# Kernel optimization log

Hardware: AMD Instinct MI355X
Metric: run time of the kernel (lower is better)

## Reference

```python
import jax, jax.numpy as jnp
import numpy as np

B, T, V, E, H = 256, 512, 50000, 300, 128
NORM_GAIN = 0.8     # norm_gain fed at train time
FORGET_BIAS = 1.0
EPS = 1e-12         # tf.contrib.layers.layer_norm default epsilon


def setup_inputs() -> dict:
    key = jax.random.key(0)
    k1, k2, k3 = jax.random.split(key, 3)
    x = jax.random.randint(k1, (B, T), 0, V, dtype=jnp.int32)
    embed = jax.random.normal(k2, (V, E), dtype=jnp.float32)  # tf.random_normal stddev=1
    W = jax.random.normal(k3, (E + H, 4 * H), dtype=jnp.float32) / np.float32(np.sqrt(E + H))
    gains = jnp.full((5, H), NORM_GAIN, dtype=jnp.float32)   # i, j, f, o, cell-transform
    shifts = jnp.zeros((5, H), dtype=jnp.float32)
    return {"x": x, "embed": embed, "W": W, "gains": gains, "shifts": shifts}


def _ln(v, g, b):
    # layer norm over feature axis with learned gain/shift
    m = jnp.mean(v, axis=-1, keepdims=True)
    var = jnp.mean(jnp.square(v - m), axis=-1, keepdims=True)
    return (v - m) * jax.lax.rsqrt(var + EPS) * g + b


def reference(x, embed, W, gains, shifts):
    # embedding: einsum('abc,cd->abd', one_hot(x), embed) == embed[x]
    xe = jnp.take(embed, x, axis=0)            # [B, T, E]
    xe = jnp.transpose(xe, (1, 0, 2))          # [T, B, E] for scan
    c0 = jnp.zeros((x.shape[0], H), jnp.float32)
    h0 = c0

    def step(carry, x_t):
        c, h = carry
        z = jnp.concatenate([x_t, h], axis=-1) @ W      # [B, 4H], no bias
        i, j, f, o = jnp.split(z, 4, axis=-1)
        i = _ln(i, gains[0], shifts[0])
        j = _ln(j, gains[1], shifts[1])
        f = _ln(f, gains[2], shifts[2])
        o = _ln(o, gains[3], shifts[3])
        g = jax.nn.relu(j)                              # activation=tf.nn.relu
        new_c = c * jax.nn.sigmoid(f + FORGET_BIAS) + jax.nn.sigmoid(i) * g
        new_h = jax.nn.relu(_ln(new_c, gains[4], shifts[4])) * jax.nn.sigmoid(o)
        return (new_c, new_h), new_h

    _, ys = jax.lax.scan(step, (c0, h0), xe)            # ys: [T, B, H]
    return jnp.transpose(ys, (1, 0, 2))                 # [B, T, H]
```

## Files before the change

### kernel.cpp

```cpp
#include <hip/hip_runtime.h>
#include <math.h>

#define Bb   256
#define Tt   512
#define Vv   50000
#define Ee   300
#define Hh   128
#define G4   512
#define EPS  1e-12f
#define FBIAS 1.0f

typedef _Float16 half8 __attribute__((ext_vector_type(8)));
typedef float    f32x4 __attribute__((ext_vector_type(4)));

template <int CTRL>
__device__ inline float dpp_mov(float v) {
    return __int_as_float(
        __builtin_amdgcn_update_dpp(0, __float_as_int(v), CTRL, 0xF, 0xF, true));
}
__device__ inline float red16(float v) {
    v += dpp_mov<0xB1>(v);
    v += dpp_mov<0x4E>(v);
    v += dpp_mov<0x141>(v);
    v += dpp_mov<0x140>(v);
    return v;
}
__device__ inline float red64b(float v) {
    v = red16(v);
    v += dpp_mov<0x142>(v);
    v += dpp_mov<0x143>(v);
    return __int_as_float(__builtin_amdgcn_readlane(__float_as_int(v), 63));
}

__device__ inline void lds_barrier() {
    __builtin_amdgcn_sched_barrier(0);
    asm volatile("s_waitcnt lgkmcnt(0)" ::: "memory");
    __builtin_amdgcn_sched_barrier(0);
    __builtin_amdgcn_s_barrier();
    __builtin_amdgcn_sched_barrier(0);
}

__device__ inline float sigm(float v) {
    return __fdividef(1.0f, 1.0f + __expf(-v));
}

#define PROJ_TILES ((Vv + 31) / 32)

__global__ __launch_bounds__(512, 2) void embed_proj_mfma(
    const float* __restrict__ embed,
    const float* __restrict__ W,
    float* __restrict__ P)
{
    __shared__ __align__(16) _Float16 A[32 * 320];

    const int tid  = threadIdx.x;
    const int wv   = tid >> 6;
    const int lane = tid & 63;
    const int p16  = lane & 15;
    const int gq   = lane >> 4;

    half8 bf[4][10];
    #pragma unroll
    for (int tt = 0; tt < 4; ++tt) {
        #pragma unroll
        for (int ks = 0; ks < 10; ++ks) {
            half8 h;
            #pragma unroll
            for (int j = 0; j < 8; ++j) {
                int k = ks * 32 + gq * 8 + j;
                h[j] = (k < Ee)
                     ? (_Float16)W[(size_t)k * G4 + wv * 64 + tt * 16 + p16]
                     : (_Float16)0.f;
            }
            bf[tt][ks] = h;
        }
    }

    char* const Ab = (char*)A;
    for (int i = tid; i < 32 * 10; i += 512) {
        int row = i / 10, m = i - row * 10;
        *(uint*)(Ab + ((row * 640 + 600 + m * 4) ^ ((row & 7) << 4))) = 0u;
    }
    __syncthreads();

    for (int mtile = blockIdx.x; mtile < PROJ_TILES; mtile += gridDim.x) {
        const int r0 = mtile * 32;

        for (int i = tid; i < 32 * 75; i += 512) {
            int row = i / 75, k4 = i - row * 75;
            int grow = r0 + row;
            float4 v = (grow < Vv) ? *(const float4*)&embed[(size_t)grow * Ee + k4 * 4]
                                   : (float4){0.f, 0.f, 0.f, 0.f};
            union { _Float16 h[4]; uint2 u; } pk;
            pk.h[0] = (_Float16)v.x; pk.h[1] = (_Float16)v.y;
            pk.h[2] = (_Float16)v.z; pk.h[3] = (_Float16)v.w;
            *(uint2*)(Ab + ((row * 640 + k4 * 8) ^ ((row & 7) << 4))) = pk.u;
        }
        __syncthreads();

        f32x4 acc[2][4];
        #pragma unroll
        for (int mt = 0; mt < 2; ++mt)
            #pragma unroll
            for (int tt = 0; tt < 4; ++tt)
                acc[mt][tt] = (f32x4){0.f, 0.f, 0.f, 0.f};

        #pragma unroll
        for (int mt = 0; mt < 2; ++mt) {
            const int arow = mt * 16 + p16;
            #pragma unroll
            for (int ks = 0; ks < 10; ++ks) {
                half8 af = *(const half8*)(Ab + ((arow * 640 + ks * 64 + gq * 16)
                                                 ^ ((arow & 7) << 4)));
                #pragma unroll
                for (int tt = 0; tt < 4; ++tt)
                    acc[mt][tt] = __builtin_amdgcn_mfma_f32_16x16x32_f16(
                        af, bf[tt][ks], acc[mt][tt], 0, 0, 0);
            }
        }

        #pragma unroll
        for (int mt = 0; mt < 2; ++mt)
            #pragma unroll
            for (int tt = 0; tt < 4; ++tt)
                #pragma unroll
                for (int r = 0; r < 4; ++r) {
                    int row = r0 + mt * 16 + gq * 4 + r;
                    if (row < Vv)
                        P[(size_t)row * G4 + wv * 64 + tt * 16 + p16] = acc[mt][tt][r];
                }
        __syncthreads();
    }
}

#define RPBLK 4
#define LBLK  (Bb / RPBLK)

#define LSTM_STEP(TSTEP, PC, PN)                                               \
{                                                                              \
                      \
    {                                                                          \
        int tn   = ((TSTEP) + 1 < Tt) ? (TSTEP) + 1 : Tt - 1;                  \
        int tokn = xrow[tn];                                                   \
        _Pragma("unroll")                                                      \
        for (int g = 0; g < 4; ++g)                                            \
            PN[g] = *(const float2*)&P[(size_t)tokn * G4 + g * 128 + 2 * lane];\
    }                                                                          \
    {                                                                          \
        half8 af[4];                                                           \
        _Pragma("unroll")                                                      \
        for (int ks = 0; ks < 4; ++ks)                                         \
            af[ks] = *(const half8*)(hb + p16 * 256 +                          \
                         ((ks * 64 + (gq << 4)) ^ ((p16 & 7) << 4)));          \
        f32x4 acc[8];                                                          \
        _Pragma("unroll")                                                      \
        for (int tt = 0; tt < 8; ++tt) acc[tt] = (f32x4){0.f, 0.f, 0.f, 0.f};  \
        _Pragma("unroll")                                                      \
        for (int tt = 0; tt < 8; ++tt) {                                       \
            _Pragma("unroll")                                                  \
            for (int ks = 0; ks < 4; ++ks)                                     \
                acc[tt] = __builtin_amdgcn_mfma_f32_16x16x32_f16(              \
                    af[ks], bfrag[tt][ks], acc[tt], 0, 0, 0);                  \
        }                                                                      \
        if (lane < 16) {                                                       \
            _Pragma("unroll")                                                  \
            for (int g = 0; g < 4; ++g) {                                      \
                _Pragma("unroll")                                              \
                for (int hh = 0; hh < 2; ++hh) {                               \
                    const int tt  = g * 2 + hh;                                \
                    const int col = g * 128 + wv * 32 + hh * 16 + p16;         \
                    _Pragma("unroll")                                          \
                    for (int r = 0; r < 4; ++r) z_lds[r][col] = acc[tt][r];    \
                }                                                              \
            }                                                                  \
        }                                                                      \
    }                                                                          \
    lds_barrier();                                               \
          \
    {                                                                          \
        float2 zi[4];                                                          \
        _Pragma("unroll")                                                      \
        for (int g = 0; g < 4; ++g) {                                          \
            float2 zr = *(const float2*)&z_lds[wv][g * 128 + 2 * lane];        \
            zi[g].x = zr.x + PC[g].x;                                          \
            zi[g].y = zr.y + PC[g].y;                                          \
        }                                                                      \
        float mean[4], rstd[4];                                                \
        _Pragma("unroll")                                                      \
        for (int g = 0; g < 4; ++g) {                                          \
            float s = red64b(zi[g].x + zi[g].y);                               \
            float q = red64b(fmaf(zi[g].x, zi[g].x, zi[g].y * zi[g].y));       \
            mean[g] = s * (1.0f / Hh);                                         \
            float var = q * (1.0f / Hh) - mean[g] * mean[g];                   \
            rstd[g] = rsqrtf(var + EPS);                                       \
        }                                                                      \
        float2 nv[4];                                                          \
        _Pragma("unroll")                                                      \
        for (int g = 0; g < 4; ++g) {                                          \
            nv[g].x = (zi[g].x - mean[g]) * rstd[g] * gg[g].x + sg[g].x;       \
            nv[g].y = (zi[g].y - mean[g]) * rstd[g] * gg[g].y + sg[g].y;       \
        }                                                                      \
        c0 = c0 * sigm(nv[2].x + FBIAS) + sigm(nv[0].x) * fmaxf(nv[1].x, 0.f); \
        c1 = c1 * sigm(nv[2].y + FBIAS) + sigm(nv[0].y) * fmaxf(nv[1].y, 0.f); \
        float s2 = red64b(c0 + c1);                                            \
        float q2 = red64b(fmaf(c0, c0, c1 * c1));                              \
        const float m2 = s2 * (1.0f / Hh);                                     \
        const float v2 = q2 * (1.0f / Hh) - m2 * m2;                           \
        const float r2 = rsqrtf(v2 + EPS);                                     \
        const float lc0 = (c0 - m2) * r2 * gcell.x + scell.x;                  \
        const float lc1 = (c1 - m2) * r2 * gcell.y + scell.y;                  \
        const float h0 = fmaxf(lc0, 0.f) * sigm(nv[3].x);                      \
        const float h1 = fmaxf(lc1, 0.f) * sigm(nv[3].y);                      \
        {                                                                      \
            union { _Float16 hh2[2]; uint u; } pk;                             \
            pk.hh2[0] = (_Float16)h0; pk.hh2[1] = (_Float16)h1;                \
            *(uint*)(hb + wv * 256 + ((4 * lane) ^ ((wv & 7) << 4))) = pk.u;   \
        }                                                                      \
        *(float2*)&out[((size_t)row_g * Tt + (TSTEP)) * Hh + 2 * lane] =       \
            (float2){h0, h1};                                                  \
    }                                                                          \
    lds_barrier();                                                \
}

__global__ __launch_bounds__(256, 1) void lstm_mfma4(
    const float* __restrict__ P,
    const float* __restrict__ W,
    const int*   __restrict__ x,
    const float* __restrict__ gains,
    const float* __restrict__ shifts,
    float* __restrict__ out)
{
    __shared__ __align__(16) float    z_lds[RPBLK][G4];
    __shared__ __align__(16) _Float16 h_lds[16][Hh];

    const int tid  = threadIdx.x;
    const int wv   = tid >> 6;
    const int lane = tid & 63;
    const int gq   = lane >> 4;
    const int p16  = lane & 15;
    const int bb   = blockIdx.x;

    {
        uint* hz = (uint*)h_lds;
        #pragma unroll
        for (int i = 0; i < 4; ++i) hz[tid + 256 * i] = 0u;
    }

    half8 bfrag[8][4];
    #pragma unroll
    for (int g = 0; g < 4; ++g) {
        #pragma unroll
        for (int hh = 0; hh < 2; ++hh) {
            #pragma unroll
            for (int ks = 0; ks < 4; ++ks) {
                half8 h;
                #pragma unroll
                for (int j = 0; j < 8; ++j) {
                    h[j] = (_Float16)W[(size_t)(Ee + ks * 32 + gq * 8 + j) * G4
                                       + g * 128 + wv * 32 + hh * 16 + p16];
                }
                bfrag[g * 2 + hh][ks] = h;
            }
        }
    }

    float2 gg[4], sg[4];
    #pragma unroll
    for (int g = 0; g < 4; ++g) {
        gg[g] = *(const float2*)&gains[g * Hh + 2 * lane];
        sg[g] = *(const float2*)&shifts[g * Hh + 2 * lane];
    }
    const float2 gcell = *(const float2*)&gains[4 * Hh + 2 * lane];
    const float2 scell = *(const float2*)&shifts[4 * Hh + 2 * lane];

    const int  row_g = bb * RPBLK + wv;
    const int* xrow  = x + (size_t)row_g * Tt;

    float c0 = 0.f, c1 = 0.f;

    float2 pA[4], pB[4];
    {
        int tok0 = xrow[0];
        #pragma unroll
        for (int g = 0; g < 4; ++g)
            pA[g] = *(const float2*)&P[(size_t)tok0 * G4 + g * 128 + 2 * lane];
    }

    char* const hb = (char*)h_lds;

    __syncthreads();

    for (int t = 0; t < Tt; t += 2) {
        LSTM_STEP(t,     pA, pB)
        LSTM_STEP(t + 1, pB, pA)
    }
}

extern "C" void kernel_launch(void* const* d_in, const int* in_sizes, int n_in,
                              void* d_out, int out_size, void* d_ws, size_t ws_size,
                              hipStream_t stream) {
    const int*   x      = (const int*)d_in[0];
    const float* embed  = (const float*)d_in[1];
    const float* W      = (const float*)d_in[2];
    const float* gains  = (const float*)d_in[3];
    const float* shifts = (const float*)d_in[4];
    float* out = (float*)d_out;

    float* P = (float*)d_ws;

    embed_proj_mfma<<<dim3(256), dim3(512), 0, stream>>>(embed, W, P);
    lstm_mfma4<<<dim3(LBLK), dim3(256), 0, stream>>>(P, W, x, gains, shifts, out);
}
```

Measured before the change: 826.7 us.

## Store input projection in fp16, stage tokens in LDS, prefetch two steps ahead

The embedding-projection table P is now written in fp16, which halves both its write traffic and the per-step gather reads in the recurrent kernel. Each block copies its token ids into shared memory up front, so the token lookup no longer touches global memory inside the recurrence. The P rows are prefetched two steps ahead using a three-buffer rotation, which hides gather latency behind more work. The cost is extra rounding on the precomputed input projection and more register and LDS use.

```diff
diff --git a/kernel.cpp b/kernel.cpp
--- a/kernel.cpp
+++ b/kernel.cpp
@@ -49,7 +49,7 @@
 __global__ __launch_bounds__(512, 2) void embed_proj_mfma(
     const float* __restrict__ embed,
     const float* __restrict__ W,
-    float* __restrict__ P)
+    _Float16* __restrict__ P)
 {
     __shared__ __align__(16) _Float16 A[32 * 320];
 
@@ -127,7 +127,8 @@
                 for (int r = 0; r < 4; ++r) {
                     int row = r0 + mt * 16 + gq * 4 + r;
                     if (row < Vv)
-                        P[(size_t)row * G4 + wv * 64 + tt * 16 + p16] = acc[mt][tt][r];
+                        P[(size_t)row * G4 + wv * 64 + tt * 16 + p16] =
+                            (_Float16)acc[mt][tt][r];
                 }
         __syncthreads();
     }
@@ -136,15 +137,14 @@
 #define RPBLK 4
 #define LBLK  (Bb / RPBLK)
 
-#define LSTM_STEP(TSTEP, PC, PN)                                               \
+#define LSTM_STEP(TSTEP, PC, PL)                                               \
 {                                                                              \
-                      \
+              \
     {                                                                          \
-        int tn   = ((TSTEP) + 1 < Tt) ? (TSTEP) + 1 : Tt - 1;                  \
-        int tokn = xrow[tn];                                                   \
+        const _Float16* pr = P + (size_t)tkR * G4;                             \
         _Pragma("unroll")                                                      \
         for (int g = 0; g < 4; ++g)                                            \
-            PN[g] = *(const float2*)&P[(size_t)tokn * G4 + g * 128 + 2 * lane];\
+            PL[g] = *(const uint*)&pr[g * 128 + 2 * lane];                     \
     }                                                                          \
     {                                                                          \
         half8 af[4];                                                           \
@@ -178,12 +178,14 @@
     lds_barrier();                                               \
           \
     {                                                                          \
+        tkR = xtok[wv][((TSTEP) + 3 < Tt) ? (TSTEP) + 3 : Tt - 1];             \
         float2 zi[4];                                                          \
         _Pragma("unroll")                                                      \
         for (int g = 0; g < 4; ++g) {                                          \
+            union { uint u; _Float16 h[2]; } pk; pk.u = PC[g];                 \
             float2 zr = *(const float2*)&z_lds[wv][g * 128 + 2 * lane];        \
-            zi[g].x = zr.x + PC[g].x;                                          \
-            zi[g].y = zr.y + PC[g].y;                                          \
+            zi[g].x = zr.x + (float)pk.h[0];                                   \
+            zi[g].y = zr.y + (float)pk.h[1];                                   \
         }                                                                      \
         float mean[4], rstd[4];                                                \
         _Pragma("unroll")                                                      \
@@ -222,8 +224,8 @@
     lds_barrier();                                                \
 }
 
-__global__ __launch_bounds__(256, 1) void lstm_mfma4(
-    const float* __restrict__ P,
+__global__ __launch_bounds__(256, 1) void lstm_mfma5(
+    const _Float16* __restrict__ P,
     const float* __restrict__ W,
     const int*   __restrict__ x,
     const float* __restrict__ gains,
@@ -232,6 +234,7 @@
 {
     __shared__ __align__(16) float    z_lds[RPBLK][G4];
     __shared__ __align__(16) _Float16 h_lds[16][Hh];
+    __shared__ __align__(16) int      xtok[RPBLK][Tt];
 
     const int tid  = threadIdx.x;
     const int wv   = tid >> 6;
@@ -239,6 +242,12 @@
     const int gq   = lane >> 4;
     const int p16  = lane & 15;
     const int bb   = blockIdx.x;
+
+    {
+        const int4* xs = (const int4*)(x + (size_t)bb * RPBLK * Tt);
+        int4* xd = (int4*)&xtok[0][0];
+        for (int i = tid; i < 512; i += 256) xd[i] = xs[i];
+    }
 
     {
         uint* hz = (uint*)h_lds;
@@ -273,27 +282,35 @@
     const float2 gcell = *(const float2*)&gains[4 * Hh + 2 * lane];
     const float2 scell = *(const float2*)&shifts[4 * Hh + 2 * lane];
 
-    const int  row_g = bb * RPBLK + wv;
-    const int* xrow  = x + (size_t)row_g * Tt;
+    const int row_g = bb * RPBLK + wv;
 
     float c0 = 0.f, c1 = 0.f;
-
-    float2 pA[4], pB[4];
+    char* const hb = (char*)h_lds;
+
+    __syncthreads();
+
+    uint pA[4], pB[4], pC[4];
+    int tkR;
     {
-        int tok0 = xrow[0];
-        #pragma unroll
-        for (int g = 0; g < 4; ++g)
-            pA[g] = *(const float2*)&P[(size_t)tok0 * G4 + g * 128 + 2 * lane];
-    }
-
-    char* const hb = (char*)h_lds;
-
-    __syncthreads();
-
-    for (int t = 0; t < Tt; t += 2) {
-        LSTM_STEP(t,     pA, pB)
+        int tk0 = xtok[wv][0];
+        int tk1 = xtok[wv][1];
+        tkR = xtok[wv][2];
+        const _Float16* p0 = P + (size_t)tk0 * G4;
+        const _Float16* p1 = P + (size_t)tk1 * G4;
+        #pragma unroll
+        for (int g = 0; g < 4; ++g) {
+            pA[g] = *(const uint*)&p0[g * 128 + 2 * lane];
+            pB[g] = *(const uint*)&p1[g * 128 + 2 * lane];
+        }
+    }
+
+    for (int t = 0; t < 510; t += 3) {
+        LSTM_STEP(t,     pA, pC)
         LSTM_STEP(t + 1, pB, pA)
-    }
+        LSTM_STEP(t + 2, pC, pB)
+    }
+    LSTM_STEP(510, pA, pC)
+    LSTM_STEP(511, pB, pA)
 }
 
 extern "C" void kernel_launch(void* const* d_in, const int* in_sizes, int n_in,
@@ -306,8 +323,8 @@
     const float* shifts = (const float*)d_in[4];
     float* out = (float*)d_out;
 
-    float* P = (float*)d_ws;
+    _Float16* P = (_Float16*)d_ws;
 
     embed_proj_mfma<<<dim3(256), dim3(512), 0, stream>>>(embed, W, P);
-    lstm_mfma4<<<dim3(LBLK), dim3(256), 0, stream>>>(P, W, x, gains, shifts, out);
-}
+    lstm_mfma5<<<dim3(LBLK), dim3(256), 0, stream>>>(P, W, x, gains, shifts, out);
+}
```

Result: faster. 794.2 us (-3.9%).

## Split LSTM gate matmul across eight waves with fp16 projection table and fused LN stats

Applied to the files above, without the earlier changes.

The recurrent kernel now runs 512 threads per block, so each of eight waves computes one 64-column gate slice of the h·W product. The per-token input projection is injected directly as the MFMA accumulator initializer, and the projection table is stored as fp16 to halve gather bandwidth. Layer-norm sums and sums of squares are computed from the accumulators and shared via a small LDS partial buffer, which replaces the cross-lane reductions for the four gates. Tokens are staged in LDS, gathers are prefetched two steps ahead, and sched barriers are removed around the block barrier. The cost is lower precision in the projection, extra LDS traffic, and only half the waves doing the elementwise phase.

```diff
diff --git a/kernel.cpp b/kernel.cpp
--- a/kernel.cpp
+++ b/kernel.cpp
@@ -33,11 +33,8 @@
 }
 
 __device__ inline void lds_barrier() {
-    __builtin_amdgcn_sched_barrier(0);
     asm volatile("s_waitcnt lgkmcnt(0)" ::: "memory");
-    __builtin_amdgcn_sched_barrier(0);
     __builtin_amdgcn_s_barrier();
-    __builtin_amdgcn_sched_barrier(0);
 }
 
 __device__ inline float sigm(float v) {
@@ -49,7 +46,7 @@
 __global__ __launch_bounds__(512, 2) void embed_proj_mfma(
     const float* __restrict__ embed,
     const float* __restrict__ W,
-    float* __restrict__ P)
+    _Float16* __restrict__ P)
 {
     __shared__ __align__(16) _Float16 A[32 * 320];
 
@@ -127,7 +124,8 @@
                 for (int r = 0; r < 4; ++r) {
                     int row = r0 + mt * 16 + gq * 4 + r;
                     if (row < Vv)
-                        P[(size_t)row * G4 + wv * 64 + tt * 16 + p16] = acc[mt][tt][r];
+                        P[(size_t)row * G4 + wv * 64 + tt * 16 + p16] =
+                            (_Float16)acc[mt][tt][r];
                 }
         __syncthreads();
     }
@@ -136,70 +134,121 @@
 #define RPBLK 4
 #define LBLK  (Bb / RPBLK)
 
-#define LSTM_STEP(TSTEP, PC, PN)                                               \
+#define PLOAD(PM, TI)                                                          \
 {                                                                              \
-                      \
-    {                                                                          \
-        int tn   = ((TSTEP) + 1 < Tt) ? (TSTEP) + 1 : Tt - 1;                  \
-        int tokn = xrow[tn];                                                   \
-        _Pragma("unroll")                                                      \
-        for (int g = 0; g < 4; ++g)                                            \
-            PN[g] = *(const float2*)&P[(size_t)tokn * G4 + g * 128 + 2 * lane];\
+    const int ti_ = (TI) < Tt ? (TI) : Tt - 1;                                 \
+    const int a0 = xtok[0][ti_], a1 = xtok[1][ti_];                            \
+    const int a2 = xtok[2][ti_], a3 = xtok[3][ti_];                            \
+    const unsigned short* Pu = (const unsigned short*)P;                       \
+    const unsigned short* b0 = Pu + (size_t)a0 * G4 + wv * 64 + p16;           \
+    const unsigned short* b1 = Pu + (size_t)a1 * G4 + wv * 64 + p16;           \
+    const unsigned short* b2 = Pu + (size_t)a2 * G4 + wv * 64 + p16;           \
+    const unsigned short* b3 = Pu + (size_t)a3 * G4 + wv * 64 + p16;           \
+    _Pragma("unroll")                                                          \
+    for (int tt = 0; tt < 4; ++tt) {                                           \
+        PM[0 * 4 + tt] = b0[tt * 16];                                          \
+        PM[1 * 4 + tt] = b1[tt * 16];                                          \
+        PM[2 * 4 + tt] = b2[tt * 16];                                          \
+        PM[3 * 4 + tt] = b3[tt * 16];                                          \
     }                                                                          \
+}
+
+#define LSTM_STEP(TSTEP, PM)                                                   \
+{                                                                              \
+    \
     {                                                                          \
         half8 af[4];                                                           \
         _Pragma("unroll")                                                      \
         for (int ks = 0; ks < 4; ++ks)                                         \
             af[ks] = *(const half8*)(hb + p16 * 256 +                          \
                          ((ks * 64 + (gq << 4)) ^ ((p16 & 7) << 4)));          \
-        f32x4 acc[8];                                                          \
-        _Pragma("unroll")                                                      \
-        for (int tt = 0; tt < 8; ++tt) acc[tt] = (f32x4){0.f, 0.f, 0.f, 0.f};  \
-        _Pragma("unroll")                                                      \
-        for (int tt = 0; tt < 8; ++tt) {                                       \
+        f32x4 acc[4];                                                          \
+        _Pragma("unroll")                                                      \
+        for (int tt = 0; tt < 4; ++tt) {                                       \
+            f32x4 a;                                                           \
+            _Pragma("unroll")                                                  \
+            for (int r = 0; r < 4; ++r) {                                      \
+                unsigned short u = (unsigned short)PM[r * 4 + tt];             \
+                float pv = (float)__builtin_bit_cast(_Float16, u);             \
+                a[r] = (lane < 16) ? pv : 0.f;                                 \
+            }                                                                  \
+            acc[tt] = a;                                                       \
+        }                                                                      \
+        _Pragma("unroll")                                                      \
+        for (int tt = 0; tt < 4; ++tt) {                                       \
             _Pragma("unroll")                                                  \
             for (int ks = 0; ks < 4; ++ks)                                     \
                 acc[tt] = __builtin_amdgcn_mfma_f32_16x16x32_f16(              \
                     af[ks], bfrag[tt][ks], acc[tt], 0, 0, 0);                  \
         }                                                                      \
+                   \
+        PLOAD(PM, (TSTEP) + 2)                                                 \
+                                       \
         if (lane < 16) {                                                       \
             _Pragma("unroll")                                                  \
-            for (int g = 0; g < 4; ++g) {                                      \
+            for (int tt = 0; tt < 4; ++tt) {                                   \
+                const int col = wv * 64 + tt * 16 + p16;                       \
                 _Pragma("unroll")                                              \
-                for (int hh = 0; hh < 2; ++hh) {                               \
-                    const int tt  = g * 2 + hh;                                \
-                    const int col = g * 128 + wv * 32 + hh * 16 + p16;         \
-                    _Pragma("unroll")                                          \
-                    for (int r = 0; r < 4; ++r) z_lds[r][col] = acc[tt][r];    \
-                }                                                              \
+                for (int r = 0; r < 4; ++r) z_lds[r][col] = acc[tt][r];        \
             }                                                                  \
         }                                                                      \
+                 \
+        {                                                                      \
+            float sA[4], qA[4];                                                \
+            _Pragma("unroll")                                                  \
+            for (int r = 0; r < 4; ++r) {                                      \
+                float s = (acc[0][r] + acc[1][r]) + (acc[2][r] + acc[3][r]);   \
+                float q = acc[0][r] * acc[0][r];                               \
+                q = fmaf(acc[1][r], acc[1][r], q);                             \
+                q = fmaf(acc[2][r], acc[2][r], q);                             \
+                q = fmaf(acc[3][r], acc[3][r], q);                             \
+                sA[r] = red16(s); qA[r] = red16(q);                            \
+            }                                                                  \
+            float ws = sA[0], wq = qA[0];                                      \
+            ws = (p16 == 1) ? sA[1] : ws;  wq = (p16 == 1) ? qA[1] : wq;       \
+            ws = (p16 == 2) ? sA[2] : ws;  wq = (p16 == 2) ? qA[2] : wq;       \
+            ws = (p16 == 3) ? sA[3] : ws;  wq = (p16 == 3) ? qA[3] : wq;       \
+            if (lane < 4) *(float2*)&part[lane][wv][0] = (float2){ws, wq};     \
+        }                                                                      \
     }                                                                          \
-    lds_barrier();                                               \
-          \
-    {                                                                          \
+    lds_barrier();                                    \
+             \
+    if (wv < 4) {                                                              \
         float2 zi[4];                                                          \
         _Pragma("unroll")                                                      \
+        for (int g = 0; g < 4; ++g)                                            \
+            zi[g] = *(const float2*)&z_lds[wv][g * 128 + 2 * lane];            \
+        const float4 pt0 = *(const float4*)&part[wv][0][0];                    \
+        const float4 pt1 = *(const float4*)&part[wv][2][0];                    \
+        const float4 pt2 = *(const float4*)&part[wv][4][0];                    \
+        const float4 pt3 = *(const float4*)&part[wv][6][0];                    \
+        float mean[4], rstd[4];                                                \
+        {                                                                      \
+            float st, qt;                                                      \
+            st = pt0.x + pt0.z; qt = pt0.y + pt0.w;                            \
+            mean[0] = st * (1.0f / Hh);                                        \
+            rstd[0] = rsqrtf(qt * (1.0f / Hh) - mean[0] * mean[0] + EPS);      \
+            st = pt1.x + pt1.z; qt = pt1.y + pt1.w;                            \
+            mean[1] = st * (1.0f / Hh);                                        \
+            rstd[1] = rsqrtf(qt * (1.0f / Hh) - mean[1] * mean[1] + EPS);      \
+            st = pt2.x + pt2.z; qt = pt2.y + pt2.w;                            \
+            mean[2] = st * (1.0f / Hh);                                        \
+            rstd[2] = rsqrtf(qt * (1.0f / Hh) - mean[2] * mean[2] + EPS);      \
+            st = pt3.x + pt3.z; qt = pt3.y + pt3.w;                            \
+            mean[3] = st * (1.0f / Hh);                                        \
+            rstd[3] = rsqrtf(qt * (1.0f / Hh) - mean[3] * mean[3] + EPS);      \
+        }                                                                      \
+        float2 nv[4];                                                          \
+        _Pragma("unroll")                                                      \
         for (int g = 0; g < 4; ++g) {                                          \
-            float2 zr = *(const float2*)&z_lds[wv][g * 128 + 2 * lane];        \
-            zi[g].x = zr.x + PC[g].x;                                          \
-            zi[g].y = zr.y + PC[g].y;                                          \
-        }                                                                      \
-        float mean[4], rstd[4];                                                \
-        _Pragma("unroll")                                                      \
-        for (int g = 0; g < 4; ++g) {                                          \
-            float s = red64b(zi[g].x + zi[g].y);                               \
-            float q = red64b(fmaf(zi[g].x, zi[g].x, zi[g].y * zi[g].y));       \
-            mean[g] = s * (1.0f / Hh);                                         \
-            float var = q * (1.0f / Hh) - mean[g] * mean[g];                   \
-            rstd[g] = rsqrtf(var + EPS);                                       \
-        }                                                                      \
-        float2 nv[4];                                                          \
-        _Pragma("unroll")                                                      \
-        for (int g = 0; g < 4; ++g) {                                          \
-            nv[g].x = (zi[g].x - mean[g]) * rstd[g] * gg[g].x + sg[g].x;       \
-            nv[g].y = (zi[g].y - mean[g]) * rstd[g] * gg[g].y + sg[g].y;       \
-        }                                                                      \
+            const float ax = rstd[g] * gg[g].x, ay = rstd[g] * gg[g].y;        \
+            const float bx = sg[g].x - mean[g] * ax;                           \
+            const float by = sg[g].y - mean[g] * ay;                           \
+            nv[g].x = fmaf(zi[g].x, ax, bx);                                   \
+            nv[g].y = fmaf(zi[g].y, ay, by);                                   \
+        }                                                                      \
+        const float sox = sigm(nv[3].x);                                       \
+        const float soy = sigm(nv[3].y);                                       \
         c0 = c0 * sigm(nv[2].x + FBIAS) + sigm(nv[0].x) * fmaxf(nv[1].x, 0.f); \
         c1 = c1 * sigm(nv[2].y + FBIAS) + sigm(nv[0].y) * fmaxf(nv[1].y, 0.f); \
         float s2 = red64b(c0 + c1);                                            \
@@ -209,8 +258,8 @@
         const float r2 = rsqrtf(v2 + EPS);                                     \
         const float lc0 = (c0 - m2) * r2 * gcell.x + scell.x;                  \
         const float lc1 = (c1 - m2) * r2 * gcell.y + scell.y;                  \
-        const float h0 = fmaxf(lc0, 0.f) * sigm(nv[3].x);                      \
-        const float h1 = fmaxf(lc1, 0.f) * sigm(nv[3].y);                      \
+        const float h0 = fmaxf(lc0, 0.f) * sox;                                \
+        const float h1 = fmaxf(lc1, 0.f) * soy;                                \
         {                                                                      \
             union { _Float16 hh2[2]; uint u; } pk;                             \
             pk.hh2[0] = (_Float16)h0; pk.hh2[1] = (_Float16)h1;                \
@@ -222,8 +271,8 @@
     lds_barrier();                                                \
 }
 
-__global__ __launch_bounds__(256, 1) void lstm_mfma4(
-    const float* __restrict__ P,
+__global__ __launch_bounds__(512, 1) void lstm_mfma8(
+    const _Float16* __restrict__ P,
     const float* __restrict__ W,
     const int*   __restrict__ x,
     const float* __restrict__ gains,
@@ -232,6 +281,8 @@
 {
     __shared__ __align__(16) float    z_lds[RPBLK][G4];
     __shared__ __align__(16) _Float16 h_lds[16][Hh];
+    __shared__ __align__(16) int      xtok[RPBLK][Tt];
+    __shared__ __align__(16) float    part[RPBLK][8][2];
 
     const int tid  = threadIdx.x;
     const int wv   = tid >> 6;
@@ -241,26 +292,26 @@
     const int bb   = blockIdx.x;
 
     {
+        const int4* xs = (const int4*)(x + (size_t)bb * RPBLK * Tt);
+        ((int4*)&xtok[0][0])[tid] = xs[tid];
+    }
+    {
         uint* hz = (uint*)h_lds;
-        #pragma unroll
-        for (int i = 0; i < 4; ++i) hz[tid + 256 * i] = 0u;
-    }
-
-    half8 bfrag[8][4];
+        hz[tid] = 0u; hz[tid + 512] = 0u;
+    }
+
+    half8 bfrag[4][4];
     #pragma unroll
-    for (int g = 0; g < 4; ++g) {
-        #pragma unroll
-        for (int hh = 0; hh < 2; ++hh) {
-            #pragma unroll
-            for (int ks = 0; ks < 4; ++ks) {
-                half8 h;
-                #pragma unroll
-                for (int j = 0; j < 8; ++j) {
-                    h[j] = (_Float16)W[(size_t)(Ee + ks * 32 + gq * 8 + j) * G4
-                                       + g * 128 + wv * 32 + hh * 16 + p16];
-                }
-                bfrag[g * 2 + hh][ks] = h;
+    for (int tt = 0; tt < 4; ++tt) {
+        #pragma unroll
+        for (int ks = 0; ks < 4; ++ks) {
+            half8 h;
+            #pragma unroll
+            for (int j = 0; j < 8; ++j) {
+                h[j] = (_Float16)W[(size_t)(Ee + ks * 32 + gq * 8 + j) * G4
+                                   + wv * 64 + tt * 16 + p16];
             }
+            bfrag[tt][ks] = h;
         }
     }
 
@@ -273,26 +324,20 @@
     const float2 gcell = *(const float2*)&gains[4 * Hh + 2 * lane];
     const float2 scell = *(const float2*)&shifts[4 * Hh + 2 * lane];
 
-    const int  row_g = bb * RPBLK + wv;
-    const int* xrow  = x + (size_t)row_g * Tt;
+    const int row_g = bb * RPBLK + (wv & 3);
 
     float c0 = 0.f, c1 = 0.f;
-
-    float2 pA[4], pB[4];
-    {
-        int tok0 = xrow[0];
-        #pragma unroll
-        for (int g = 0; g < 4; ++g)
-            pA[g] = *(const float2*)&P[(size_t)tok0 * G4 + g * 128 + 2 * lane];
-    }
-
     char* const hb = (char*)h_lds;
 
     __syncthreads();
 
+    uint pmA[16], pmB[16];
+    PLOAD(pmA, 0)
+    PLOAD(pmB, 1)
+
     for (int t = 0; t < Tt; t += 2) {
-        LSTM_STEP(t,     pA, pB)
-        LSTM_STEP(t + 1, pB, pA)
+        LSTM_STEP(t,     pmA)
+        LSTM_STEP(t + 1, pmB)
     }
 }
 
@@ -306,8 +351,8 @@
     const float* shifts = (const float*)d_in[4];
     float* out = (float*)d_out;
 
-    float* P = (float*)d_ws;
+    _Float16* P = (_Float16*)d_ws;
 
     embed_proj_mfma<<<dim3(256), dim3(512), 0, stream>>>(embed, W, P);
-    lstm_mfma4<<<dim3(LBLK), dim3(256), 0, stream>>>(P, W, x, gains, shifts, out);
-}
+    lstm_mfma8<<<dim3(LBLK), dim3(512), 0, stream>>>(P, W, x, gains, shifts, out);
+}
```

After: 855.7 us. 1.04x slower.
